# Kernel tuning notes

Measured on AMD Instinct MI355X. Metric: run time of the kernel, lower is better.

Reference implementation:

```python
import jax, jax.numpy as jnp
from jax import lax
import numpy as np

N_NEURON = 4096
BATCH = 64
N_STEP = 200


def setup_inputs() -> dict:
    key = jax.random.key(0)
    k1, k2, k3 = jax.random.split(key, 3)
    # state_g is a sigmoid output: keep strictly inside (0, 1) for g_inverse's log
    state_g = jax.random.uniform(k1, (BATCH, N_NEURON), dtype=jnp.float32,
                                 minval=0.05, maxval=0.95)
    # Symmetric_Linear init: W ~ N(0, 0.01), symmetrized, zero diagonal
    W = jax.random.normal(k2, (N_NEURON, N_NEURON), dtype=jnp.float32) * 0.01
    W = W + W.T
    W = W - jnp.diag(jnp.diag(W))
    b = jax.random.normal(k3, (N_NEURON,), dtype=jnp.float32) * 0.01
    beta = jnp.ones((N_NEURON,), dtype=jnp.float32) * 10.0
    tau = jnp.ones((N_NEURON,), dtype=jnp.float32)
    dt_train = jnp.float32(0.1)
    return {"state_g": state_g, "W": W, "b": b, "beta": beta, "tau": tau,
            "dt_train": dt_train, "n_step": N_STEP}


def reference(state_g, W, b, beta, tau, dt_train, n_step):
    # max_x = 50 / beta.max()  (original uses .item(); beta is constant so same value)
    max_x = 50.0 / jnp.max(beta)
    # Symmetric_Linear effective weight: (W + W^T)/2 with zero diagonal.
    # Original recomputes this every step; it's step-invariant so hoist it.
    W_sym = (W + W.T) * 0.5 - jnp.diag(jnp.diag(W))
    # g_inverse: x = (1/beta) * log(g / (1 - g))
    state_x = (1.0 / beta) * jnp.log(state_g / (1.0 - state_g))
    alpha = dt_train / tau  # [N]

    def step(carry, _):
        x, g = carry
        pre = g @ W_sym.T + b                       # [B, N] GEMM
        x = alpha * pre + (1.0 - alpha) * x         # leaky update
        x = jnp.clip(x, -max_x, max_x)
        g = jax.nn.sigmoid(beta * x)
        return (x, g), None

    (state_x, state_g), _ = lax.scan(step, (state_x, state_g), None, length=n_step)
    return state_g
```

## Files before the change

kernel.cpp:

```cpp
#include <hip/hip_runtime.h>
#include <hip/hip_bf16.h>

#define MM 64
#define NN 4096
#define KK 4096
#define NSTEP 200
#define NSLICE 8
#define NSTRIP 32
#define NPART 8

typedef __bf16 bf16x8 __attribute__((ext_vector_type(8)));
typedef float  f32x4  __attribute__((ext_vector_type(4)));

static __device__ __forceinline__ unsigned short f2bf(float f) {
    __hip_bfloat16 h = __float2bfloat16(f);
    return __builtin_bit_cast(unsigned short, h);
}
static __device__ __forceinline__ float bf2f(unsigned short u) {
    __hip_bfloat16 h = __builtin_bit_cast(__hip_bfloat16, u);
    return __bfloat162float(h);
}


__global__ __launch_bounds__(256) void symm_kernel(const float* __restrict__ W,
                                                   unsigned short* __restrict__ Wfh,
                                                   unsigned short* __restrict__ Wfl) {
    __shared__ float T[64][65];
    const int tid = threadIdx.x;
    const int r0 = blockIdx.y * 64, c0 = blockIdx.x * 64;
#pragma unroll
    for (int i = 0; i < 4; ++i) {
        int lin = tid + i * 256;
        int cc  = lin >> 4;
        int r4  = (lin & 15) * 4;
        float4 v = *(const float4*)&W[(size_t)(c0 + cc) * NN + r0 + r4];
        T[cc][r4 + 0] = v.x; T[cc][r4 + 1] = v.y;
        T[cc][r4 + 2] = v.z; T[cc][r4 + 3] = v.w;
    }
    __syncthreads();
#pragma unroll
    for (int i = 0; i < 4; ++i) {
        int lin = tid + i * 256;
        int rr  = lin >> 4;
        int c4  = (lin & 15) * 4;
        float4 v = *(const float4*)&W[(size_t)(r0 + rr) * NN + c0 + c4];
        float d[4] = {v.x, v.y, v.z, v.w};
        ushort4 ohi, olo;
        unsigned short* ph = (unsigned short*)&ohi;
        unsigned short* pl = (unsigned short*)&olo;
#pragma unroll
        for (int j = 0; j < 4; ++j) {
            float sv = 0.5f * (d[j] + T[c4 + j][rr]);
            if (r0 + rr == c0 + c4 + j) sv = 0.0f;
            unsigned short hi = f2bf(sv);
            ph[j] = hi;
            pl[j] = f2bf(sv - bf2f(hi));
        }
        const int n  = r0 + rr;
        const int kg = c0 + c4;
        const int s_ = n >> 7, ns = (n >> 4) & 7, ln = n & 15;
        const int kc = kg >> 5, q = (kg & 31) >> 3, j0 = kg & 7;
        size_t off = ((((size_t)(s_ * 8 + ns) * 128 + kc) * 64 + q * 16 + ln)) * 8 + j0;
        *(ushort4*)&Wfh[off] = ohi;
        *(ushort4*)&Wfl[off] = olo;
    }
}

__global__ __launch_bounds__(256) void init_kernel(const float* __restrict__ g_in,
                                                   const float* __restrict__ beta,
                                                   float* __restrict__ x,
                                                   unsigned short* __restrict__ gfh,
                                                   unsigned short* __restrict__ gfl) {
    int idx = blockIdx.x * 256 + threadIdx.x;
    int r = idx >> 12, c = idx & (NN - 1);
    float g = g_in[idx];
    x[idx] = logf(g / (1.0f - g)) / beta[c];
    unsigned short hi = f2bf(g);
    unsigned short lo = f2bf(g - bf2f(hi));
    size_t off = (((size_t)(c >> 5) * 4 + (r >> 4)) * 64 + ((c & 31) >> 3) * 16 + (r & 15)) * 8 + (c & 7);
    gfh[off] = hi;
    gfl[off] = lo;
}

__global__ __launch_bounds__(256) void maxx_kernel(const float* __restrict__ beta,
                                                   float* __restrict__ out) {
    __shared__ float red[256];
    float m = -1e30f;
    for (int i = threadIdx.x; i < NN; i += 256) m = fmaxf(m, beta[i]);
    red[threadIdx.x] = m;
    __syncthreads();
    for (int s = 128; s > 0; s >>= 1) {
        if (threadIdx.x < s) red[threadIdx.x] = fmaxf(red[threadIdx.x], red[threadIdx.x + s]);
        __syncthreads();
    }
    if (threadIdx.x == 0) out[0] = 50.0f / red[0];
}

__global__ __launch_bounds__(1024, 1) void gemm_kernel(
    const unsigned short* __restrict__ gfh,
    const unsigned short* __restrict__ gfl,
    const unsigned short* __restrict__ Wfh,
    const unsigned short* __restrict__ Wfl,
    float* __restrict__ P)
{
    __shared__ float sacc[12][32][64];

    const int tid  = threadIdx.x;
    const int w    = tid >> 6;
    const int lane = tid & 63;
    const int q    = lane >> 4;
    const int l16  = lane & 15;

    const int s = blockIdx.x >> 3;
    const int k = blockIdx.x & 7;

    const int mh = w & 1;
    const int nh = (w >> 1) & 1;
    const int kh = w >> 2;

    f32x4 acc[2][4] = {};

#pragma unroll
    for (int it = 0; it < 4; ++it) {
        const int kc = k * 16 + kh * 4 + it;
        const size_t aBase = ((size_t)kc * 4) * 512 + lane * 8;
        const size_t bBase = (((size_t)(s * 8) * 128 + kc) * 64 + lane) * 8;
        bf16x8 ah[2], al[2], bh[4], bl[4];
#pragma unroll
        for (int mi = 0; mi < 2; ++mi) {
            const size_t a = aBase + (size_t)(mh * 2 + mi) * 512;
            ah[mi] = *(const bf16x8*)&gfh[a];
            al[mi] = *(const bf16x8*)&gfl[a];
        }
#pragma unroll
        for (int ni = 0; ni < 4; ++ni) {
            const size_t b = bBase + (size_t)(nh * 4 + ni) * 128 * 512;
            bh[ni] = *(const bf16x8*)&Wfh[b];
            bl[ni] = *(const bf16x8*)&Wfl[b];
        }
#pragma unroll
        for (int mi = 0; mi < 2; ++mi)
#pragma unroll
            for (int ni = 0; ni < 4; ++ni) {
                acc[mi][ni] = __builtin_amdgcn_mfma_f32_16x16x32_bf16(ah[mi], bh[ni], acc[mi][ni], 0, 0, 0);
                acc[mi][ni] = __builtin_amdgcn_mfma_f32_16x16x32_bf16(al[mi], bh[ni], acc[mi][ni], 0, 0, 0);
                acc[mi][ni] = __builtin_amdgcn_mfma_f32_16x16x32_bf16(ah[mi], bl[ni], acc[mi][ni], 0, 0, 0);
            }
    }

    if (kh > 0) {
#pragma unroll
        for (int mi = 0; mi < 2; ++mi)
#pragma unroll
            for (int ni = 0; ni < 4; ++ni)
#pragma unroll
                for (int rg = 0; rg < 4; ++rg)
                    sacc[w - 4][(mi * 4 + ni) * 4 + rg][lane] = acc[mi][ni][rg];
    }
    __syncthreads();
    if (kh == 0) {
        float* Pb = &P[((size_t)(k * NSTRIP + s) * 64) * 128];
#pragma unroll
        for (int mi = 0; mi < 2; ++mi)
#pragma unroll
            for (int ni = 0; ni < 4; ++ni)
#pragma unroll
                for (int rg = 0; rg < 4; ++rg) {
                    const int idx = (mi * 4 + ni) * 4 + rg;
                    const int row = mh * 32 + mi * 16 + q * 4 + rg;
                    const int col = nh * 64 + ni * 16 + l16;
                    float v = acc[mi][ni][rg]
                            + sacc[w][idx][lane]
                            + sacc[w + 4][idx][lane]
                            + sacc[w + 8][idx][lane];
                    Pb[(size_t)row * 128 + col] = v;
                }
    }
}

__global__ __launch_bounds__(256) void epi_kernel(
    const float* __restrict__ P,
    float* __restrict__ x,
    unsigned short* __restrict__ gfh_out,
    unsigned short* __restrict__ gfl_out,
    const float* __restrict__ bvec,
    const float* __restrict__ beta,
    const float* __restrict__ tau,
    const float* __restrict__ dt_ptr,
    const float* __restrict__ maxx_ptr,
    float* __restrict__ gout_f32)
{
    const int t  = blockIdx.x * 256 + threadIdx.x;
    const int m  = t >> 9;
    const int n0 = (t & 511) * 8;
    const int s  = n0 >> 7;

    float sum[8] = {};
#pragma unroll
    for (int k = 0; k < NPART; ++k) {
        const float* p = &P[((size_t)(k * NSTRIP + s) * 64 + m) * 128 + (n0 & 127)];
        float4 p0 = *(const float4*)&p[0];
        float4 p1 = *(const float4*)&p[4];
        sum[0] += p0.x; sum[1] += p0.y; sum[2] += p0.z; sum[3] += p0.w;
        sum[4] += p1.x; sum[5] += p1.y; sum[6] += p1.z; sum[7] += p1.w;
    }

    const float dt = *dt_ptr;
    const float mx = *maxx_ptr;
    float4 b0 = *(const float4*)&bvec[n0], b1 = *(const float4*)&bvec[n0 + 4];
    float4 e0 = *(const float4*)&beta[n0], e1 = *(const float4*)&beta[n0 + 4];
    float4 t0 = *(const float4*)&tau[n0],  t1 = *(const float4*)&tau[n0 + 4];
    float bb[8] = {b0.x, b0.y, b0.z, b0.w, b1.x, b1.y, b1.z, b1.w};
    float be[8] = {e0.x, e0.y, e0.z, e0.w, e1.x, e1.y, e1.z, e1.w};
    float tv[8] = {t0.x, t0.y, t0.z, t0.w, t1.x, t1.y, t1.z, t1.w};

    float* xp = &x[(size_t)m * NN + n0];
    float4 x0 = *(const float4*)&xp[0], x1 = *(const float4*)&xp[4];
    float xo[8] = {x0.x, x0.y, x0.z, x0.w, x1.x, x1.y, x1.z, x1.w};

    float gg[8];
    unsigned short vh[8], vl[8];
#pragma unroll
    for (int j = 0; j < 8; ++j) {
        const float al = dt / tv[j];
        float xn = al * (sum[j] + bb[j]) + (1.0f - al) * xo[j];
        xn = fminf(fmaxf(xn, -mx), mx);
        float g = 1.0f / (1.0f + __expf(-be[j] * xn));
        xo[j] = xn;
        gg[j] = g;
        unsigned short hi = f2bf(g);
        vh[j] = hi;
        vl[j] = f2bf(g - bf2f(hi));
    }
    *(float4*)&xp[0] = {xo[0], xo[1], xo[2], xo[3]};
    *(float4*)&xp[4] = {xo[4], xo[5], xo[6], xo[7]};

    size_t off = (((size_t)(n0 >> 5) * 4 + (m >> 4)) * 64 + ((n0 & 31) >> 3) * 16 + (m & 15)) * 8;
    *(ushort4*)&gfh_out[off]     = {vh[0], vh[1], vh[2], vh[3]};
    *(ushort4*)&gfh_out[off + 4] = {vh[4], vh[5], vh[6], vh[7]};
    *(ushort4*)&gfl_out[off]     = {vl[0], vl[1], vl[2], vl[3]};
    *(ushort4*)&gfl_out[off + 4] = {vl[4], vl[5], vl[6], vl[7]};

    if (gout_f32) {
        *(float4*)&gout_f32[(size_t)m * NN + n0]     = {gg[0], gg[1], gg[2], gg[3]};
        *(float4*)&gout_f32[(size_t)m * NN + n0 + 4] = {gg[4], gg[5], gg[6], gg[7]};
    }
}

extern "C" void kernel_launch(void* const* d_in, const int* in_sizes, int n_in,
                              void* d_out, int out_size, void* d_ws, size_t ws_size,
                              hipStream_t stream) {
    const float* state_g = (const float*)d_in[0];
    const float* W       = (const float*)d_in[1];
    const float* b       = (const float*)d_in[2];
    const float* beta    = (const float*)d_in[3];
    const float* tau     = (const float*)d_in[4];
    const float* dt      = (const float*)d_in[5];
    float* out = (float*)d_out;

    char* ws = (char*)d_ws;
    const size_t WH = (size_t)KK * NN * 2;
    const size_t XB = (size_t)MM * NN * 4;
    const size_t GB = (size_t)MM * NN * 2;
    const size_t PB = (size_t)NPART * NSTRIP * 64 * 128 * 4;
    unsigned short* Wfh = (unsigned short*)ws;
    unsigned short* Wfl = (unsigned short*)(ws + WH);
    float*          x   = (float*)(ws + 2 * WH);
    unsigned short* g0h = (unsigned short*)(ws + 2 * WH + XB);
    unsigned short* g0l = (unsigned short*)(ws + 2 * WH + XB + GB);
    unsigned short* g1h = (unsigned short*)(ws + 2 * WH + XB + 2 * GB);
    unsigned short* g1l = (unsigned short*)(ws + 2 * WH + XB + 3 * GB);
    float*          P   = (float*)(ws + 2 * WH + XB + 4 * GB);
    float*          mxp = (float*)(ws + 2 * WH + XB + 4 * GB + PB);

    symm_kernel<<<dim3(64, 64), 256, 0, stream>>>(W, Wfh, Wfl);
    init_kernel<<<(MM * NN) / 256, 256, 0, stream>>>(state_g, beta, x, g0h, g0l);
    maxx_kernel<<<1, 256, 0, stream>>>(beta, mxp);

    unsigned short *gih = g0h, *gil = g0l, *goh = g1h, *gol = g1l;
    for (int st = 0; st < NSTEP; ++st) {
        float* of = (st == NSTEP - 1) ? out : nullptr;
        gemm_kernel<<<NSTRIP * NSLICE, 1024, 0, stream>>>(gih, gil, Wfh, Wfl, P);
        epi_kernel<<<128, 256, 0, stream>>>(P, x, goh, gol, b, beta, tau, dt, mxp, of);
        unsigned short* tp;
        tp = gih; gih = goh; goh = tp;
        tp = gil; gil = gol; gol = tp;
    }
}
```

Before: 3.818 ms.

## Fuse GEMM and epilogue into one per-step kernel with in-block K reduction

Replaces the split-K GEMM plus separate epilogue kernel with a single step kernel. Each block owns a 16-column strip of N across all of K, with 16 waves splitting K and reducing through shared memory before applying the leaky update and sigmoid in-block. This removes the partial-sum buffer round trip through global memory and one kernel launch per step. The W layout is changed to 16-column strips to match. In exchange, each wave now reuses one B fragment across four A fragments, so more A traffic is loaded per block, and only 256 of 1024 threads run the epilogue.

Result: slower. 4.213 ms (+10.3%).

```diff
diff --git a/kernel.cpp b/kernel.cpp
--- a/kernel.cpp
+++ b/kernel.cpp
@@ -5,9 +5,6 @@
 #define NN 4096
 #define KK 4096
 #define NSTEP 200
-#define NSLICE 8
-#define NSTRIP 32
-#define NPART 8
 
 typedef __bf16 bf16x8 __attribute__((ext_vector_type(8)));
 typedef float  f32x4  __attribute__((ext_vector_type(4)));
@@ -58,9 +55,9 @@
         }
         const int n  = r0 + rr;
         const int kg = c0 + c4;
-        const int s_ = n >> 7, ns = (n >> 4) & 7, ln = n & 15;
+        const int s16 = n >> 4, ln = n & 15;
         const int kc = kg >> 5, q = (kg & 31) >> 3, j0 = kg & 7;
-        size_t off = ((((size_t)(s_ * 8 + ns) * 128 + kc) * 64 + q * 16 + ln)) * 8 + j0;
+        size_t off = (((size_t)s16 * 128 + kc) * 64 + q * 16 + ln) * 8 + j0;
         *(ushort4*)&Wfh[off] = ohi;
         *(ushort4*)&Wfl[off] = olo;
     }
@@ -96,90 +93,11 @@
     if (threadIdx.x == 0) out[0] = 50.0f / red[0];
 }
 
-__global__ __launch_bounds__(1024, 1) void gemm_kernel(
+__global__ __launch_bounds__(1024, 1) void step_kernel(
     const unsigned short* __restrict__ gfh,
     const unsigned short* __restrict__ gfl,
     const unsigned short* __restrict__ Wfh,
     const unsigned short* __restrict__ Wfl,
-    float* __restrict__ P)
-{
-    __shared__ float sacc[12][32][64];
-
-    const int tid  = threadIdx.x;
-    const int w    = tid >> 6;
-    const int lane = tid & 63;
-    const int q    = lane >> 4;
-    const int l16  = lane & 15;
-
-    const int s = blockIdx.x >> 3;
-    const int k = blockIdx.x & 7;
-
-    const int mh = w & 1;
-    const int nh = (w >> 1) & 1;
-    const int kh = w >> 2;
-
-    f32x4 acc[2][4] = {};
-
-#pragma unroll
-    for (int it = 0; it < 4; ++it) {
-        const int kc = k * 16 + kh * 4 + it;
-        const size_t aBase = ((size_t)kc * 4) * 512 + lane * 8;
-        const size_t bBase = (((size_t)(s * 8) * 128 + kc) * 64 + lane) * 8;
-        bf16x8 ah[2], al[2], bh[4], bl[4];
-#pragma unroll
-        for (int mi = 0; mi < 2; ++mi) {
-            const size_t a = aBase + (size_t)(mh * 2 + mi) * 512;
-            ah[mi] = *(const bf16x8*)&gfh[a];
-            al[mi] = *(const bf16x8*)&gfl[a];
-        }
-#pragma unroll
-        for (int ni = 0; ni < 4; ++ni) {
-            const size_t b = bBase + (size_t)(nh * 4 + ni) * 128 * 512;
-            bh[ni] = *(const bf16x8*)&Wfh[b];
-            bl[ni] = *(const bf16x8*)&Wfl[b];
-        }
-#pragma unroll
-        for (int mi = 0; mi < 2; ++mi)
-#pragma unroll
-            for (int ni = 0; ni < 4; ++ni) {
-                acc[mi][ni] = __builtin_amdgcn_mfma_f32_16x16x32_bf16(ah[mi], bh[ni], acc[mi][ni], 0, 0, 0);
-                acc[mi][ni] = __builtin_amdgcn_mfma_f32_16x16x32_bf16(al[mi], bh[ni], acc[mi][ni], 0, 0, 0);
-                acc[mi][ni] = __builtin_amdgcn_mfma_f32_16x16x32_bf16(ah[mi], bl[ni], acc[mi][ni], 0, 0, 0);
-            }
-    }
-
-    if (kh > 0) {
-#pragma unroll
-        for (int mi = 0; mi < 2; ++mi)
-#pragma unroll
-            for (int ni = 0; ni < 4; ++ni)
-#pragma unroll
-                for (int rg = 0; rg < 4; ++rg)
-                    sacc[w - 4][(mi * 4 + ni) * 4 + rg][lane] = acc[mi][ni][rg];
-    }
-    __syncthreads();
-    if (kh == 0) {
-        float* Pb = &P[((size_t)(k * NSTRIP + s) * 64) * 128];
-#pragma unroll
-        for (int mi = 0; mi < 2; ++mi)
-#pragma unroll
-            for (int ni = 0; ni < 4; ++ni)
-#pragma unroll
-                for (int rg = 0; rg < 4; ++rg) {
-                    const int idx = (mi * 4 + ni) * 4 + rg;
-                    const int row = mh * 32 + mi * 16 + q * 4 + rg;
-                    const int col = nh * 64 + ni * 16 + l16;
-                    float v = acc[mi][ni][rg]
-                            + sacc[w][idx][lane]
-                            + sacc[w + 4][idx][lane]
-                            + sacc[w + 8][idx][lane];
-                    Pb[(size_t)row * 128 + col] = v;
-                }
-    }
-}
-
-__global__ __launch_bounds__(256) void epi_kernel(
-    const float* __restrict__ P,
     float* __restrict__ x,
     unsigned short* __restrict__ gfh_out,
     unsigned short* __restrict__ gfl_out,
@@ -190,60 +108,98 @@
     const float* __restrict__ maxx_ptr,
     float* __restrict__ gout_f32)
 {
-    const int t  = blockIdx.x * 256 + threadIdx.x;
-    const int m  = t >> 9;
-    const int n0 = (t & 511) * 8;
-    const int s  = n0 >> 7;
-
-    float sum[8] = {};
-#pragma unroll
-    for (int k = 0; k < NPART; ++k) {
-        const float* p = &P[((size_t)(k * NSTRIP + s) * 64 + m) * 128 + (n0 & 127)];
-        float4 p0 = *(const float4*)&p[0];
-        float4 p1 = *(const float4*)&p[4];
-        sum[0] += p0.x; sum[1] += p0.y; sum[2] += p0.z; sum[3] += p0.w;
-        sum[4] += p1.x; sum[5] += p1.y; sum[6] += p1.z; sum[7] += p1.w;
-    }
-
-    const float dt = *dt_ptr;
-    const float mx = *maxx_ptr;
-    float4 b0 = *(const float4*)&bvec[n0], b1 = *(const float4*)&bvec[n0 + 4];
-    float4 e0 = *(const float4*)&beta[n0], e1 = *(const float4*)&beta[n0 + 4];
-    float4 t0 = *(const float4*)&tau[n0],  t1 = *(const float4*)&tau[n0 + 4];
-    float bb[8] = {b0.x, b0.y, b0.z, b0.w, b1.x, b1.y, b1.z, b1.w};
-    float be[8] = {e0.x, e0.y, e0.z, e0.w, e1.x, e1.y, e1.z, e1.w};
-    float tv[8] = {t0.x, t0.y, t0.z, t0.w, t1.x, t1.y, t1.z, t1.w};
-
-    float* xp = &x[(size_t)m * NN + n0];
-    float4 x0 = *(const float4*)&xp[0], x1 = *(const float4*)&xp[4];
-    float xo[8] = {x0.x, x0.y, x0.z, x0.w, x1.x, x1.y, x1.z, x1.w};
-
-    float gg[8];
-    unsigned short vh[8], vl[8];
-#pragma unroll
-    for (int j = 0; j < 8; ++j) {
-        const float al = dt / tv[j];
-        float xn = al * (sum[j] + bb[j]) + (1.0f - al) * xo[j];
-        xn = fminf(fmaxf(xn, -mx), mx);
-        float g = 1.0f / (1.0f + __expf(-be[j] * xn));
-        xo[j] = xn;
-        gg[j] = g;
-        unsigned short hi = f2bf(g);
-        vh[j] = hi;
-        vl[j] = f2bf(g - bf2f(hi));
-    }
-    *(float4*)&xp[0] = {xo[0], xo[1], xo[2], xo[3]};
-    *(float4*)&xp[4] = {xo[4], xo[5], xo[6], xo[7]};
-
-    size_t off = (((size_t)(n0 >> 5) * 4 + (m >> 4)) * 64 + ((n0 & 31) >> 3) * 16 + (m & 15)) * 8;
-    *(ushort4*)&gfh_out[off]     = {vh[0], vh[1], vh[2], vh[3]};
-    *(ushort4*)&gfh_out[off + 4] = {vh[4], vh[5], vh[6], vh[7]};
-    *(ushort4*)&gfl_out[off]     = {vl[0], vl[1], vl[2], vl[3]};
-    *(ushort4*)&gfl_out[off + 4] = {vl[4], vl[5], vl[6], vl[7]};
-
-    if (gout_f32) {
-        *(float4*)&gout_f32[(size_t)m * NN + n0]     = {gg[0], gg[1], gg[2], gg[3]};
-        *(float4*)&gout_f32[(size_t)m * NN + n0 + 4] = {gg[4], gg[5], gg[6], gg[7]};
+    __shared__ float sacc[16][16][65];
+
+    const int tid  = threadIdx.x;
+    const int w    = tid >> 6;
+    const int lane = tid & 63;
+    const int s16  = blockIdx.x;
+
+    f32x4 acc[4] = {};
+
+#pragma unroll 2
+    for (int it = 0; it < 8; ++it) {
+        const int kc = w * 8 + it;
+        const size_t aBase = (size_t)kc * 2048 + lane * 8;
+        const size_t bOff  = ((size_t)s16 * 128 + kc) * 512 + lane * 8;
+        bf16x8 bh = *(const bf16x8*)&Wfh[bOff];
+        bf16x8 bl = *(const bf16x8*)&Wfl[bOff];
+        bf16x8 ah[4], al[4];
+#pragma unroll
+        for (int mq = 0; mq < 4; ++mq) {
+            ah[mq] = *(const bf16x8*)&gfh[aBase + (size_t)mq * 512];
+            al[mq] = *(const bf16x8*)&gfl[aBase + (size_t)mq * 512];
+        }
+#pragma unroll
+        for (int mq = 0; mq < 4; ++mq) {
+            acc[mq] = __builtin_amdgcn_mfma_f32_16x16x32_bf16(ah[mq], bh, acc[mq], 0, 0, 0);
+            acc[mq] = __builtin_amdgcn_mfma_f32_16x16x32_bf16(al[mq], bh, acc[mq], 0, 0, 0);
+            acc[mq] = __builtin_amdgcn_mfma_f32_16x16x32_bf16(ah[mq], bl, acc[mq], 0, 0, 0);
+        }
+    }
+
+#pragma unroll
+    for (int mq = 0; mq < 4; ++mq)
+#pragma unroll
+        for (int rg = 0; rg < 4; ++rg)
+            sacc[w][mq * 4 + rg][lane] = acc[mq][rg];
+    __syncthreads();
+
+    if (tid < 256) {
+        const int m  = tid >> 2;
+        const int qq = tid & 3;
+        const int c0 = qq * 4;
+        const int n0 = s16 * 16 + c0;
+        const int mq = m >> 4;
+        const int q  = (m & 15) >> 2;
+        const int rg = m & 3;
+        const int ridx = mq * 4 + rg;
+
+        float sum[4];
+#pragma unroll
+        for (int jj = 0; jj < 4; ++jj) {
+            float v = 0.0f;
+#pragma unroll
+            for (int kh = 0; kh < 16; ++kh)
+                v += sacc[kh][ridx][q * 16 + c0 + jj];
+            sum[jj] = v;
+        }
+
+        const float dt = *dt_ptr;
+        const float mx = *maxx_ptr;
+        float4 b0 = *(const float4*)&bvec[n0];
+        float4 e0 = *(const float4*)&beta[n0];
+        float4 t0 = *(const float4*)&tau[n0];
+        float bb[4] = {b0.x, b0.y, b0.z, b0.w};
+        float be[4] = {e0.x, e0.y, e0.z, e0.w};
+        float tv[4] = {t0.x, t0.y, t0.z, t0.w};
+
+        float* xp = &x[(size_t)m * NN + n0];
+        float4 x0 = *(const float4*)xp;
+        float xo[4] = {x0.x, x0.y, x0.z, x0.w};
+
+        float gg[4];
+        unsigned short vh[4], vl[4];
+#pragma unroll
+        for (int j = 0; j < 4; ++j) {
+            const float al = dt / tv[j];
+            float xn = al * (sum[j] + bb[j]) + (1.0f - al) * xo[j];
+            xn = fminf(fmaxf(xn, -mx), mx);
+            float g = 1.0f / (1.0f + __expf(-be[j] * xn));
+            xo[j] = xn;
+            gg[j] = g;
+            unsigned short hi = f2bf(g);
+            vh[j] = hi;
+            vl[j] = f2bf(g - bf2f(hi));
+        }
+        *(float4*)xp = {xo[0], xo[1], xo[2], xo[3]};
+
+        size_t off = (((size_t)(n0 >> 5) * 4 + (m >> 4)) * 64 + ((n0 & 31) >> 3) * 16 + (m & 15)) * 8 + (n0 & 7);
+        *(ushort4*)&gfh_out[off] = {vh[0], vh[1], vh[2], vh[3]};
+        *(ushort4*)&gfl_out[off] = {vl[0], vl[1], vl[2], vl[3]};
+
+        if (gout_f32)
+            *(float4*)&gout_f32[(size_t)m * NN + n0] = {gg[0], gg[1], gg[2], gg[3]};
     }
 }
 
@@ -262,7 +218,6 @@
     const size_t WH = (size_t)KK * NN * 2;
     const size_t XB = (size_t)MM * NN * 4;
     const size_t GB = (size_t)MM * NN * 2;
-    const size_t PB = (size_t)NPART * NSTRIP * 64 * 128 * 4;
     unsigned short* Wfh = (unsigned short*)ws;
     unsigned short* Wfl = (unsigned short*)(ws + WH);
     float*          x   = (float*)(ws + 2 * WH);
@@ -270,8 +225,7 @@
     unsigned short* g0l = (unsigned short*)(ws + 2 * WH + XB + GB);
     unsigned short* g1h = (unsigned short*)(ws + 2 * WH + XB + 2 * GB);
     unsigned short* g1l = (unsigned short*)(ws + 2 * WH + XB + 3 * GB);
-    float*          P   = (float*)(ws + 2 * WH + XB + 4 * GB);
-    float*          mxp = (float*)(ws + 2 * WH + XB + 4 * GB + PB);
+    float*          mxp = (float*)(ws + 2 * WH + XB + 4 * GB);
 
     symm_kernel<<<dim3(64, 64), 256, 0, stream>>>(W, Wfh, Wfl);
     init_kernel<<<(MM * NN) / 256, 256, 0, stream>>>(state_g, beta, x, g0h, g0l);
@@ -280,8 +234,8 @@
     unsigned short *gih = g0h, *gil = g0l, *goh = g1h, *gol = g1l;
     for (int st = 0; st < NSTEP; ++st) {
         float* of = (st == NSTEP - 1) ? out : nullptr;
-        gemm_kernel<<<NSTRIP * NSLICE, 1024, 0, stream>>>(gih, gil, Wfh, Wfl, P);
-        epi_kernel<<<128, 256, 0, stream>>>(P, x, goh, gol, b, beta, tau, dt, mxp, of);
+        step_kernel<<<256, 1024, 0, stream>>>(gih, gil, Wfh, Wfl, x,
+                                              goh, gol, b, beta, tau, dt, mxp, of);
         unsigned short* tp;
         tp = gih; gih = goh; goh = tp;
         tp = gil; gil = gol; gol = tp;
```
